# Performance work log

Measured on AMD Instinct MI355X. Metric: run time of the kernel, lower is better.

## Reference

```python
import jax, jax.numpy as jnp
import numpy as np

N, E, IN_C, HID, OUT_C, HEADS, NUM_CLASSES = 50000, 800000, 128, 64, 64, 4, 40
NEG_SLOPE = 0.2


def _gat_conv(x, src, dst, W, a_src, a_dst, bias, heads, concat):
    # x: [N, F_in]; W: [F_in, heads*C]; a_src/a_dst: [1, heads, C]; bias: [out]
    n = x.shape[0]
    h = (x @ W).reshape(n, heads, -1)                      # [N, H, C]
    alpha_s = (h * a_src).sum(-1)                          # [N, H]
    alpha_d = (h * a_dst).sum(-1)                          # [N, H]
    e = jax.nn.leaky_relu(alpha_s[src] + alpha_d[dst], NEG_SLOPE)  # [E, H]
    # scatter-softmax over incoming edges of each dst node
    emax = jax.ops.segment_max(e, dst, num_segments=n)
    emax = jnp.where(jnp.isfinite(emax), emax, 0.0)
    ee = jnp.exp(e - emax[dst])
    denom = jax.ops.segment_sum(ee, dst, num_segments=n) + 1e-16
    w = ee / denom[dst]                                    # [E, H]
    out = jax.ops.segment_sum(h[src] * w[:, :, None], dst, num_segments=n)  # [N, H, C]
    out = out.reshape(n, -1) if concat else out.mean(axis=1)
    return out + bias


def setup_inputs() -> dict:
    key = jax.random.key(0)
    ks = jax.random.split(key, 12)
    s1 = 1.0 / np.sqrt(IN_C)
    s2 = 1.0 / np.sqrt(HID * HEADS)
    s3 = 1.0 / np.sqrt(OUT_C)
    return {
        "x": jax.random.normal(ks[0], (N, IN_C), dtype=jnp.float32),
        "edge_index": jax.random.randint(ks[1], (2, E), 0, N, dtype=jnp.int64),
        "W1": jax.random.normal(ks[2], (IN_C, HEADS * HID), dtype=jnp.float32) * s1,
        "att_src1": jax.random.normal(ks[3], (1, HEADS, HID), dtype=jnp.float32) * s1,
        "att_dst1": jax.random.normal(ks[4], (1, HEADS, HID), dtype=jnp.float32) * s1,
        "b1": jnp.zeros((HEADS * HID,), dtype=jnp.float32),
        "W2": jax.random.normal(ks[5], (HEADS * HID, OUT_C), dtype=jnp.float32) * s2,
        "att_src2": jax.random.normal(ks[6], (1, 1, OUT_C), dtype=jnp.float32) * s2,
        "att_dst2": jax.random.normal(ks[7], (1, 1, OUT_C), dtype=jnp.float32) * s2,
        "b2": jnp.zeros((OUT_C,), dtype=jnp.float32),
        "fc_w": jax.random.normal(ks[8], (OUT_C, NUM_CLASSES), dtype=jnp.float32) * s3,
        "fc_b": jnp.zeros((NUM_CLASSES,), dtype=jnp.float32),
    }


def reference(x, edge_index, W1, att_src1, att_dst1, b1, W2, att_src2, att_dst2, b2, fc_w, fc_b):
    n = x.shape[0]
    loops = jnp.arange(n, dtype=edge_index.dtype)
    ei = jnp.concatenate([edge_index, jnp.stack([loops, loops])], axis=1)  # add self-loops (PyG default)
    src, dst = ei[0], ei[1]
    h = jax.nn.relu(_gat_conv(x, src, dst, W1, att_src1, att_dst1, b1, HEADS, True))
    h = jax.nn.relu(_gat_conv(h, src, dst, W2, att_src2, att_dst2, b2, 1, False))
    # dropout p=0.01 is identity in eval mode
    pooled = h.mean(axis=0, keepdims=True)                 # global mean pool -> [1, OUT_C]
    logits = pooled @ fc_w + fc_b
    return jax.nn.log_softmax(logits, axis=1)
```

## Files before the change

### kernel.cpp

```cpp
#include <hip/hip_runtime.h>
#include <hip/hip_bf16.h>
#include <math.h>

#define NEG_SLOPE 0.2f
#define CHUNK2 2048
#define PGROUPS 32

typedef __attribute__((ext_vector_type(8))) short bf16x8;
typedef __attribute__((ext_vector_type(4))) float f32x4;
typedef __attribute__((ext_vector_type(2))) float f32x2_t;

__device__ __forceinline__ float lrelu(float a) { return a >= 0.f ? a : NEG_SLOPE * a; }
__device__ __forceinline__ unsigned short f2bu(float v) {
  unsigned u = __float_as_uint(v);
  u += 0x7fffu + ((u >> 16) & 1u);
  return (unsigned short)(u >> 16);
}
__device__ __forceinline__ unsigned char f2fp8(float v) {
  return (unsigned char)(__builtin_amdgcn_cvt_pk_fp8_f32(v, v, 0, false) & 0xFF);
}

__global__ __launch_bounds__(256) void prep_kernel(
    const float* __restrict__ W1, unsigned short* __restrict__ w1t,
    const float* __restrict__ W2, unsigned short* __restrict__ w2t,
    const int* __restrict__ ei, int* __restrict__ bhist,
    int E0, int Etot, int NBUCK, int wBlocks, int histBlocks) {
  __shared__ int hsm[256];
  int t = threadIdx.x;
  if (blockIdx.x < (unsigned)wBlocks) {
    const int tot1 = 128 * 256, tot2 = 256 * 64;
    for (int i = blockIdx.x * 256 + t; i < tot1 + tot2; i += wBlocks * 256) {
      if (i < tot1) { int k = i >> 8, n = i & 255; w1t[n * 128 + k] = f2bu(W1[i]); }
      else { int j = i - tot1; int k = j >> 6, n = j & 63; w2t[n * 256 + k] = f2bu(W2[j]); }
    }
  } else {
    int bid = blockIdx.x - wBlocks;
    hsm[t] = 0;
    __syncthreads();
    for (int e = bid * 256 + t; e < Etot; e += histBlocks * 256) {
      int dst = (e < E0) ? ei[E0 + e] : (e - E0);
      atomicAdd(&hsm[dst >> 8], 1);
    }
    __syncthreads();
    if (t < NBUCK && hsm[t]) atomicAdd(&bhist[t], hsm[t]);
  }
}

__global__ __launch_bounds__(256) void bucket_scan_kernel(const int* __restrict__ bhist,
    int* __restrict__ bucketOff, int* __restrict__ cursor, int* __restrict__ rowptrN,
    float* __restrict__ pooled_grp, int NBUCK, int Etot) {
  __shared__ int s[256];
  int t = threadIdx.x;
  int v = (t < NBUCK) ? bhist[t] : 0;
  s[t] = v;
  __syncthreads();
  for (int off = 1; off < 256; off <<= 1) {
    int u = (t >= off) ? s[t - off] : 0;
    __syncthreads();
    s[t] += u;
    __syncthreads();
  }
  int excl = s[t] - v;
  if (t < NBUCK) { bucketOff[t] = excl; cursor[t] = excl; }
  if (t == 0) { bucketOff[NBUCK] = Etot; *rowptrN = Etot; }
  for (int i = t; i < PGROUPS * 64; i += 256) pooled_grp[i] = 0.f;
}

__device__ void gemm1_tile(const float* __restrict__ x,
    const unsigned short* __restrict__ BT, unsigned char* __restrict__ C8,
    const float* __restrict__ att_s, const float* __restrict__ att_d,
    float* __restrict__ as_, float* __restrict__ ad_,
    int M, int by, char* smem) {
  unsigned short (*Al)[40] = (unsigned short (*)[40])smem;
  unsigned short (*Bt)[40] = (unsigned short (*)[40])(smem + 5120);
  const int tid = threadIdx.x;
  const int row0 = by * 64;
  const int lane = tid & 63, wave = tid >> 6;
  const int l15 = lane & 15, q = lane >> 4;

  f32x4 acc[4][4] = {};
  const int rr = tid >> 2, rc = (tid & 3) * 8;

  for (int k0 = 0; k0 < 128; k0 += 32) {
    float4 v0 = make_float4(0.f, 0.f, 0.f, 0.f), v1 = v0;
    if (row0 + rr < M) {
      const float* ap = x + (size_t)(row0 + rr) * 128 + k0 + rc;
      v0 = *(const float4*)ap;
      v1 = *(const float4*)(ap + 4);
    }
    *(ushort4*)&Al[rr][rc] = make_ushort4(f2bu(v0.x), f2bu(v0.y), f2bu(v0.z), f2bu(v0.w));
    *(ushort4*)&Al[rr][rc + 4] = make_ushort4(f2bu(v1.x), f2bu(v1.y), f2bu(v1.z), f2bu(v1.w));
    {
      const ushort4* bp = (const ushort4*)(BT + (size_t)tid * 128 + k0);
#pragma unroll
      for (int i = 0; i < 8; i++) *(ushort4*)&Bt[tid][i * 4] = bp[i];
    }
    __syncthreads();
    bf16x8 af[4], bf[4];
#pragma unroll
    for (int mi = 0; mi < 4; mi++)
      af[mi] = *(const bf16x8*)&Al[mi * 16 + l15][q * 8];
#pragma unroll
    for (int ni = 0; ni < 4; ni++)
      bf[ni] = *(const bf16x8*)&Bt[wave * 64 + ni * 16 + l15][q * 8];
#pragma unroll
    for (int mi = 0; mi < 4; mi++)
#pragma unroll
      for (int ni = 0; ni < 4; ni++)
        acc[mi][ni] = __builtin_amdgcn_mfma_f32_16x16x32_bf16(af[mi], bf[ni], acc[mi][ni], 0, 0, 0);
    __syncthreads();
  }
  float atts[4], attd[4];
#pragma unroll
  for (int ni = 0; ni < 4; ni++) {
    atts[ni] = att_s[wave * 64 + ni * 16 + l15];
    attd[ni] = att_d[wave * 64 + ni * 16 + l15];
  }
#pragma unroll
  for (int mi = 0; mi < 4; mi++) {
#pragma unroll
    for (int r = 0; r < 4; r++) {
      int grow = row0 + mi * 16 + q * 4 + r;
      bool ok = grow < M;
      if (ok) {
#pragma unroll
        for (int ni = 0; ni < 4; ni++)
          C8[(size_t)grow * 256 + wave * 64 + ni * 16 + l15] = f2fp8(acc[mi][ni][r]);
      }
      float vs = acc[mi][0][r] * atts[0] + acc[mi][1][r] * atts[1]
               + acc[mi][2][r] * atts[2] + acc[mi][3][r] * atts[3];
      float vd = acc[mi][0][r] * attd[0] + acc[mi][1][r] * attd[1]
               + acc[mi][2][r] * attd[2] + acc[mi][3][r] * attd[3];
#pragma unroll
      for (int off = 1; off < 16; off <<= 1) {
        vs += __shfl_xor(vs, off);
        vd += __shfl_xor(vd, off);
      }
      if (ok && l15 == 0) {
        as_[(size_t)grow * 4 + wave] = vs;
        ad_[(size_t)grow * 4 + wave] = vd;
      }
    }
  }
}

__global__ __launch_bounds__(256) void gemm1_scatter_kernel(
    const float* __restrict__ x, const unsigned short* __restrict__ BT,
    unsigned char* __restrict__ C8, const float* __restrict__ att_s,
    const float* __restrict__ att_d, float* __restrict__ as_, float* __restrict__ ad_,
    int M, const int* __restrict__ ei, int* __restrict__ cursor, int* __restrict__ pairs,
    int E0, int Etot, int NBUCK, int NSC) {
  __shared__ __align__(16) char smem[25600];
  if (blockIdx.x < (unsigned)NSC) {
    int2* stage = (int2*)smem;
    int* h = (int*)(smem + 16384);
    int* base = (int*)(smem + 17408);
    int t = threadIdx.x;
    int e0 = blockIdx.x * CHUNK2;
    h[t] = 0;
    __syncthreads();
    int cnt = Etot - e0;
    if (cnt > CHUNK2) cnt = CHUNK2;
    for (int i = t; i < cnt; i += 256) {
      int e = e0 + i;
      int s, d;
      if (e < E0) { s = ei[e]; d = ei[E0 + e]; } else { s = d = e - E0; }
      stage[i] = make_int2((s << 8) | (d & 255), d >> 8);
      atomicAdd(&h[d >> 8], 1);
    }
    __syncthreads();
    if (t < NBUCK && h[t]) base[t] = atomicAdd(&cursor[t], h[t]);
    __syncthreads();
    for (int i = t; i < cnt; i += 256) {
      int2 p = stage[i];
      int pos = atomicAdd(&base[p.y], 1);
      pairs[pos] = p.x;
    }
  } else {
    gemm1_tile(x, BT, C8, att_s, att_d, as_, ad_, M, blockIdx.x - NSC, smem);
  }
}

__global__ __launch_bounds__(256) void csr_build_kernel(const int* __restrict__ pairs,
    const int* __restrict__ bucketOff, int* __restrict__ rowptr, int* __restrict__ csr_src,
    int N) {
  int b = blockIdx.x, t = threadIdx.x;
  int base = bucketOff[b], cnt = bucketOff[b + 1] - base;
  int n0 = b << 8;
  __shared__ int h[256];
  __shared__ int s[256];
  __shared__ int ex[256];
  h[t] = 0;
  __syncthreads();
  for (int i = t; i < cnt; i += 256) atomicAdd(&h[pairs[base + i] & 255], 1);
  __syncthreads();
  int v = h[t];
  s[t] = v;
  __syncthreads();
  for (int off = 1; off < 256; off <<= 1) {
    int u = (t >= off) ? s[t - off] : 0;
    __syncthreads();
    s[t] += u;
    __syncthreads();
  }
  ex[t] = s[t] - v;
  if (n0 + t < N) rowptr[n0 + t] = base + ex[t];
  __syncthreads();
  for (int i = t; i < cnt; i += 256) {
    int p = pairs[base + i];
    int pos = atomicAdd(&ex[p & 255], 1);
    csr_src[base + pos] = ((unsigned)p) >> 8;
  }
}

#define ACCV(W, X) do {                                                        \
    f32x2_t w2_; w2_.x = (W); w2_.y = (W);                                     \
    av[0] += w2_ * __builtin_amdgcn_cvt_pk_f32_fp8((X).x, false);              \
    av[1] += w2_ * __builtin_amdgcn_cvt_pk_f32_fp8((X).x, true);               \
    av[2] += w2_ * __builtin_amdgcn_cvt_pk_f32_fp8((X).y, false);              \
    av[3] += w2_ * __builtin_amdgcn_cvt_pk_f32_fp8((X).y, true);               \
    av[4] += w2_ * __builtin_amdgcn_cvt_pk_f32_fp8((X).z, false);              \
    av[5] += w2_ * __builtin_amdgcn_cvt_pk_f32_fp8((X).z, true);               \
    av[6] += w2_ * __builtin_amdgcn_cvt_pk_f32_fp8((X).w, false);              \
    av[7] += w2_ * __builtin_amdgcn_cvt_pk_f32_fp8((X).w, true);               \
  } while (0)

__global__ __launch_bounds__(256) void aggr1_kernel(const int* __restrict__ rowptr,
    const int* __restrict__ csr_src, const float* __restrict__ as_,
    const float* __restrict__ ad_, const uint4* __restrict__ h1f8,
    const float* __restrict__ b1, unsigned short* __restrict__ out1, int Nn) {
  int lane = threadIdx.x & 63, wv = threadIdx.x >> 6;
  int q = lane >> 4, l15 = lane & 15;
  int n = (blockIdx.x * 4 + wv) * 4 + q;
  if (n >= Nn) return;
  int row = rowptr[n], deg = rowptr[n + 1] - row;
  int hh = l15 >> 2;
  float adv = ad_[n * 4 + hh];
  const uint4* hb = h1f8 + l15;
  f32x2_t av[8] = {};
  float wsum = 0.f;
  for (int s = 0; s < deg; s += 8) {
    int id[8];
    float al[8];
    uint4 xv[8];
#pragma unroll
    for (int u = 0; u < 8; u++) {
      int p = s + u;
      if (p > deg - 1) p = deg - 1;
      id[u] = csr_src[row + p];
    }
#pragma unroll
    for (int u = 0; u < 8; u++) al[u] = as_[id[u] * 4 + hh];
#pragma unroll
    for (int u = 0; u < 8; u++) xv[u] = hb[(size_t)id[u] * 16];
#pragma unroll
    for (int u = 0; u < 8; u++) {
      float w = (s + u < deg) ? __expf(lrelu(al[u] + adv)) : 0.f;
      wsum += w;
      ACCV(w, xv[u]);
    }
  }
  float vinv = 1.f / wsum;
  int c0i = l15 * 16;
  unsigned short ob[16];
#pragma unroll
  for (int k = 0; k < 4; k++) {
    float4 bb = *(const float4*)(b1 + c0i + k * 4);
    float r0 = fmaf(av[k * 2].x, vinv, bb.x);
    float r1 = fmaf(av[k * 2].y, vinv, bb.y);
    float r2 = fmaf(av[k * 2 + 1].x, vinv, bb.z);
    float r3 = fmaf(av[k * 2 + 1].y, vinv, bb.w);
    ob[k * 4 + 0] = f2bu(r0 > 0.f ? r0 : 0.f);
    ob[k * 4 + 1] = f2bu(r1 > 0.f ? r1 : 0.f);
    ob[k * 4 + 2] = f2bu(r2 > 0.f ? r2 : 0.f);
    ob[k * 4 + 3] = f2bu(r3 > 0.f ? r3 : 0.f);
  }
  *(ushort4*)(out1 + (size_t)n * 256 + c0i) = *(ushort4*)&ob[0];
  *(ushort4*)(out1 + (size_t)n * 256 + c0i + 4) = *(ushort4*)&ob[4];
  *(ushort4*)(out1 + (size_t)n * 256 + c0i + 8) = *(ushort4*)&ob[8];
  *(ushort4*)(out1 + (size_t)n * 256 + c0i + 12) = *(ushort4*)&ob[12];
}

__global__ __launch_bounds__(256) void gemm2_kernel(const unsigned short* __restrict__ A,
    const unsigned short* __restrict__ BT, unsigned char* __restrict__ C8,
    const float* __restrict__ att_s, const float* __restrict__ att_d,
    float* __restrict__ as_, float* __restrict__ ad_, int M) {
  const int K = 256, Ncol = 64;
  __shared__ __align__(16) char smem[11264];
  unsigned short (*Al)[40] = (unsigned short (*)[40])smem;
  unsigned short (*Bt)[40] = (unsigned short (*)[40])(smem + 5120);
  float* sal = (float*)(smem + 10240);
  float* sad = (float*)(smem + 10752);
  const int tid = threadIdx.x;
  const int row0 = blockIdx.x * 64;
  const int lane = tid & 63, wave = tid >> 6;
  const int wm = wave >> 1, wn = wave & 1;
  const int l15 = lane & 15, q = lane >> 4;

  f32x4 acc[2][2] = {};
  const int rr = tid >> 2, rc = (tid & 3) * 8;

  for (int k0 = 0; k0 < K; k0 += 32) {
    ushort4 av0 = make_ushort4(0, 0, 0, 0), av1 = av0;
    if (row0 + rr < M) {
      const ushort4* ap = (const ushort4*)(A + (size_t)(row0 + rr) * K + k0 + rc);
      av0 = ap[0]; av1 = ap[1];
    }
    *(ushort4*)&Al[rr][rc] = av0;
    *(ushort4*)&Al[rr][rc + 4] = av1;
    {
      const ushort4* bp = (const ushort4*)(BT + (size_t)rr * K + k0 + rc);
      *(ushort4*)&Bt[rr][rc] = bp[0];
      *(ushort4*)&Bt[rr][rc + 4] = bp[1];
    }
    __syncthreads();
    bf16x8 af[2], bf[2];
#pragma unroll
    for (int mi = 0; mi < 2; mi++)
      af[mi] = *(const bf16x8*)&Al[wm * 32 + mi * 16 + l15][q * 8];
#pragma unroll
    for (int ni = 0; ni < 2; ni++)
      bf[ni] = *(const bf16x8*)&Bt[wn * 32 + ni * 16 + l15][q * 8];
#pragma unroll
    for (int mi = 0; mi < 2; mi++)
#pragma unroll
      for (int ni = 0; ni < 2; ni++)
        acc[mi][ni] = __builtin_amdgcn_mfma_f32_16x16x32_bf16(af[mi], bf[ni], acc[mi][ni], 0, 0, 0);
    __syncthreads();
  }
#pragma unroll
  for (int mi = 0; mi < 2; mi++) {
#pragma unroll
    for (int r = 0; r < 4; r++) {
      int grow = row0 + wm * 32 + mi * 16 + q * 4 + r;
      if (grow < M) {
#pragma unroll
        for (int ni = 0; ni < 2; ni++) {
          int gcol = wn * 32 + ni * 16 + l15;
          C8[(size_t)grow * Ncol + gcol] = f2fp8(acc[mi][ni][r]);
        }
      }
    }
  }
  float atts0 = att_s[wn * 32 + l15], atts1 = att_s[wn * 32 + 16 + l15];
  float attd0 = att_d[wn * 32 + l15], attd1 = att_d[wn * 32 + 16 + l15];
#pragma unroll
  for (int mi = 0; mi < 2; mi++) {
#pragma unroll
    for (int r = 0; r < 4; r++) {
      float vs = acc[mi][0][r] * atts0 + acc[mi][1][r] * atts1;
      float vd = acc[mi][0][r] * attd0 + acc[mi][1][r] * attd1;
#pragma unroll
      for (int off = 1; off < 16; off <<= 1) {
        vs += __shfl_xor(vs, off);
        vd += __shfl_xor(vd, off);
      }
      if (l15 == 0) {
        int rl = wm * 32 + mi * 16 + q * 4 + r;
        sal[wn * 64 + rl] = vs;
        sad[wn * 64 + rl] = vd;
      }
    }
  }
  __syncthreads();
  if (tid < 64) {
    int grow = row0 + tid;
    if (grow < M) {
      as_[grow] = sal[tid] + sal[64 + tid];
      ad_[grow] = sad[tid] + sad[64 + tid];
    }
  }
}

__global__ __launch_bounds__(256) void aggr2_pool_kernel(const int* __restrict__ rowptr,
    const int* __restrict__ csr_src, const float* __restrict__ as_,
    const float* __restrict__ ad_, const unsigned* __restrict__ h2f8,
    const float* __restrict__ b2, float* __restrict__ pooled_grp, int Nn) {
  int lane = threadIdx.x & 63, wv = threadIdx.x >> 6;
  int q = lane >> 4, l15 = lane & 15;
  int c0 = l15 * 4;
  const unsigned* hb = h2f8 + l15;
  f32x2_t pv0 = {0.f, 0.f}, pv1 = {0.f, 0.f};
  int stream = (blockIdx.x * 4 + wv) * 4 + q;
  int nstreams = gridDim.x * 16;
  for (int n = stream; n < Nn; n += nstreams) {
    int row = rowptr[n], deg = rowptr[n + 1] - row;
    float adv = ad_[n];
    f32x2_t a01 = {0.f, 0.f}, a23 = {0.f, 0.f};
    float wsum = 0.f;
    for (int s = 0; s < deg; s += 8) {
      int id[8];
      float al[8];
      unsigned xv[8];
#pragma unroll
      for (int u = 0; u < 8; u++) {
        int p = s + u;
        if (p > deg - 1) p = deg - 1;
        id[u] = csr_src[row + p];
      }
#pragma unroll
      for (int u = 0; u < 8; u++) al[u] = as_[id[u]];
#pragma unroll
      for (int u = 0; u < 8; u++) xv[u] = hb[(size_t)id[u] * 16];
#pragma unroll
      for (int u = 0; u < 8; u++) {
        float w = (s + u < deg) ? __expf(lrelu(al[u] + adv)) : 0.f;
        wsum += w;
        f32x2_t w2_; w2_.x = w; w2_.y = w;
        a01 += w2_ * __builtin_amdgcn_cvt_pk_f32_fp8(xv[u], false);
        a23 += w2_ * __builtin_amdgcn_cvt_pk_f32_fp8(xv[u], true);
      }
    }
    float vinv = 1.f / wsum;
    float4 bb = *(const float4*)(b2 + c0);
    float r0 = fmaf(a01.x, vinv, bb.x), r1 = fmaf(a01.y, vinv, bb.y);
    float r2 = fmaf(a23.x, vinv, bb.z), r3 = fmaf(a23.y, vinv, bb.w);
    pv0.x += r0 > 0.f ? r0 : 0.f; pv0.y += r1 > 0.f ? r1 : 0.f;
    pv1.x += r2 > 0.f ? r2 : 0.f; pv1.y += r3 > 0.f ? r3 : 0.f;
  }
  __shared__ float4 sred[4][4][16];
  sred[wv][q][l15] = make_float4(pv0.x, pv0.y, pv1.x, pv1.y);
  __syncthreads();
  if (threadIdx.x < 64) {
    int slot = threadIdx.x >> 2, comp = threadIdx.x & 3;
    float acc = 0.f;
#pragma unroll
    for (int i = 0; i < 4; i++)
#pragma unroll
      for (int j = 0; j < 4; j++) {
        float4 v = sred[i][j][slot];
        acc += comp == 0 ? v.x : (comp == 1 ? v.y : (comp == 2 ? v.z : v.w));
      }
    atomicAdd(&pooled_grp[(blockIdx.x & (PGROUPS - 1)) * 64 + slot * 4 + comp], acc);
  }
}

__global__ __launch_bounds__(64) void pool_head_kernel(const float* __restrict__ pooled_grp,
    const float* __restrict__ fc_w, const float* __restrict__ fc_b,
    float* __restrict__ out, float invN) {
  int t = threadIdx.x;
  __shared__ float pl[64];
  __shared__ float lg[40];
  __shared__ float lse;
  float acc = 0.f;
#pragma unroll
  for (int g = 0; g < PGROUPS; g++) acc += pooled_grp[g * 64 + t];
  pl[t] = acc * invN;
  __syncthreads();
  if (t < 40) {
    float sm = fc_b[t];
    for (int c = 0; c < 64; c++) sm = fmaf(pl[c], fc_w[c * 40 + t], sm);
    lg[t] = sm;
  }
  __syncthreads();
  if (t == 0) {
    float m = -1e30f;
    for (int j = 0; j < 40; j++) m = fmaxf(m, lg[j]);
    float su = 0.f;
    for (int j = 0; j < 40; j++) su += expf(lg[j] - m);
    lse = m + logf(su);
  }
  __syncthreads();
  if (t < 40) out[t] = lg[t] - lse;
}

extern "C" void kernel_launch(void* const* d_in, const int* in_sizes, int n_in,
                              void* d_out, int out_size, void* d_ws, size_t ws_size,
                              hipStream_t stream) {
  const float* x        = (const float*)d_in[0];
  const int*   ei       = (const int*)d_in[1];
  const float* W1       = (const float*)d_in[2];
  const float* att_src1 = (const float*)d_in[3];
  const float* att_dst1 = (const float*)d_in[4];
  const float* b1       = (const float*)d_in[5];
  const float* W2       = (const float*)d_in[6];
  const float* att_src2 = (const float*)d_in[7];
  const float* att_dst2 = (const float*)d_in[8];
  const float* b2       = (const float*)d_in[9];
  const float* fc_w     = (const float*)d_in[10];
  const float* fc_b     = (const float*)d_in[11];
  float* out = (float*)d_out;

  const int N    = in_sizes[0] / 128;
  const int E0   = in_sizes[1] / 2;
  const int Etot = E0 + N;
  const int NBUCK = (N + 255) >> 8;
  const int NSC  = (Etot + CHUNK2 - 1) / CHUNK2;
  const int GBY  = (N + 63) / 64;
  const int AGG2_BLOCKS = 2048;

  char* wsb = (char*)d_ws;
  size_t o = 0;
  auto alloc = [&](size_t bytes) { char* p = wsb + o; o += (bytes + 15) & ~(size_t)15; return p; };
  unsigned short* w1t  = (unsigned short*)alloc(256 * 128 * 2);
  unsigned short* w2t  = (unsigned short*)alloc(64 * 256 * 2);
  unsigned char*  h1f8 = (unsigned char*)alloc((size_t)N * 256);
  unsigned char*  h2   = (unsigned char*)alloc((size_t)N * 64);
  unsigned short* out1 = (unsigned short*)alloc((size_t)N * 256 * 2);
  float* as1  = (float*)alloc((size_t)N * 4 * 4);
  float* ad1  = (float*)alloc((size_t)N * 4 * 4);
  float* as2  = (float*)alloc((size_t)N * 4);
  float* ad2  = (float*)alloc((size_t)N * 4);
  int* rowptr = (int*)alloc((size_t)(N + 1) * 4);
  int* bhist  = (int*)alloc(256 * 4);
  int* bucketOff = (int*)alloc(257 * 4);
  int* cursor = (int*)alloc(256 * 4);
  int* pairs  = (int*)alloc((size_t)Etot * 4);
  int* csr_src = (int*)alloc((size_t)Etot * 4);
  float* pooled_grp = (float*)alloc((size_t)PGROUPS * 64 * 4);

  dim3 blk(256);

  hipMemsetAsync(bhist, 0, 256 * sizeof(int), stream);
  prep_kernel<<<16 + 256, blk, 0, stream>>>(W1, w1t, W2, w2t, ei, bhist,
                                            E0, Etot, NBUCK, 16, 256);
  bucket_scan_kernel<<<1, blk, 0, stream>>>(bhist, bucketOff, cursor, rowptr + N,
                                            pooled_grp, NBUCK, Etot);

  gemm1_scatter_kernel<<<NSC + GBY, blk, 0, stream>>>(
      x, w1t, h1f8, att_src1, att_dst1, as1, ad1, N,
      ei, cursor, pairs, E0, Etot, NBUCK, NSC);
  csr_build_kernel<<<NBUCK, blk, 0, stream>>>(pairs, bucketOff, rowptr, csr_src, N);

  aggr1_kernel<<<(N + 15) / 16, blk, 0, stream>>>(rowptr, csr_src, as1, ad1,
                                                  (const uint4*)h1f8, b1, out1, N);

  gemm2_kernel<<<GBY, blk, 0, stream>>>(out1, w2t, h2, att_src2, att_dst2, as2, ad2, N);
  aggr2_pool_kernel<<<AGG2_BLOCKS, blk, 0, stream>>>(rowptr, csr_src, as2, ad2,
                                                     (const unsigned*)h2, b2, pooled_grp, N);

  pool_head_kernel<<<1, 64, 0, stream>>>(pooled_grp, fc_w, fc_b, out, 1.0f / (float)N);
}
```

Before: 217.0 us.

## Build CSR directly with per-node histogram and global atomic cursors

Replaces the two-level bucket sort (bucket-staged pairs followed by a per-bucket CSR build kernel) with a per-node degree histogram in the prep kernel, a per-bucket scan kernel that produces rowptr and per-node cursors, and a direct scatter of source indices into csr_src using global atomics on the destination cursor. This removes the intermediate pairs buffer and the csr_build kernel. In exchange it adds about a million global atomics on node counters in both histogram and scatter, with scattered writes, and the order of edges within each row becomes nondeterministic.

```diff
diff --git a/kernel.cpp b/kernel.cpp
--- a/kernel.cpp
+++ b/kernel.cpp
@@ -3,7 +3,6 @@
 #include <math.h>
 
 #define NEG_SLOPE 0.2f
-#define CHUNK2 2048
 #define PGROUPS 32
 
 typedef __attribute__((ext_vector_type(8))) short bf16x8;
@@ -23,7 +22,7 @@
 __global__ __launch_bounds__(256) void prep_kernel(
     const float* __restrict__ W1, unsigned short* __restrict__ w1t,
     const float* __restrict__ W2, unsigned short* __restrict__ w2t,
-    const int* __restrict__ ei, int* __restrict__ bhist,
+    const int* __restrict__ ei, int* __restrict__ bhist, int* __restrict__ nhist,
     int E0, int Etot, int NBUCK, int wBlocks, int histBlocks) {
   __shared__ int hsm[256];
   int t = threadIdx.x;
@@ -40,6 +39,7 @@
     for (int e = bid * 256 + t; e < Etot; e += histBlocks * 256) {
       int dst = (e < E0) ? ei[E0 + e] : (e - E0);
       atomicAdd(&hsm[dst >> 8], 1);
+      atomicAdd(&nhist[dst], 1);
     }
     __syncthreads();
     if (t < NBUCK && hsm[t]) atomicAdd(&bhist[t], hsm[t]);
@@ -47,7 +47,7 @@
 }
 
 __global__ __launch_bounds__(256) void bucket_scan_kernel(const int* __restrict__ bhist,
-    int* __restrict__ bucketOff, int* __restrict__ cursor, int* __restrict__ rowptrN,
+    int* __restrict__ bucketOff, int* __restrict__ rowptrN,
     float* __restrict__ pooled_grp, int NBUCK, int Etot) {
   __shared__ int s[256];
   int t = threadIdx.x;
@@ -61,9 +61,31 @@
     __syncthreads();
   }
   int excl = s[t] - v;
-  if (t < NBUCK) { bucketOff[t] = excl; cursor[t] = excl; }
+  if (t < NBUCK) bucketOff[t] = excl;
   if (t == 0) { bucketOff[NBUCK] = Etot; *rowptrN = Etot; }
   for (int i = t; i < PGROUPS * 64; i += 256) pooled_grp[i] = 0.f;
+}
+
+__global__ __launch_bounds__(256) void rowptr_kernel(const int* __restrict__ nhist,
+    const int* __restrict__ bucketOff, int* __restrict__ rowptr, int* __restrict__ cursor,
+    int N) {
+  int b = blockIdx.x, t = threadIdx.x;
+  int n = (b << 8) + t;
+  __shared__ int s[256];
+  int v = (n < N) ? nhist[n] : 0;
+  s[t] = v;
+  __syncthreads();
+  for (int off = 1; off < 256; off <<= 1) {
+    int u = (t >= off) ? s[t - off] : 0;
+    __syncthreads();
+    s[t] += u;
+    __syncthreads();
+  }
+  if (n < N) {
+    int r = bucketOff[b] + s[t] - v;
+    rowptr[n] = r;
+    cursor[n] = r;
+  }
 }
 
 __device__ void gemm1_tile(const float* __restrict__ x,
@@ -148,68 +170,18 @@
     const float* __restrict__ x, const unsigned short* __restrict__ BT,
     unsigned char* __restrict__ C8, const float* __restrict__ att_s,
     const float* __restrict__ att_d, float* __restrict__ as_, float* __restrict__ ad_,
-    int M, const int* __restrict__ ei, int* __restrict__ cursor, int* __restrict__ pairs,
-    int E0, int Etot, int NBUCK, int NSC) {
+    int M, const int* __restrict__ ei, int* __restrict__ cursor, int* __restrict__ csr_src,
+    int E0, int Etot, int NSC) {
   __shared__ __align__(16) char smem[25600];
   if (blockIdx.x < (unsigned)NSC) {
-    int2* stage = (int2*)smem;
-    int* h = (int*)(smem + 16384);
-    int* base = (int*)(smem + 17408);
-    int t = threadIdx.x;
-    int e0 = blockIdx.x * CHUNK2;
-    h[t] = 0;
-    __syncthreads();
-    int cnt = Etot - e0;
-    if (cnt > CHUNK2) cnt = CHUNK2;
-    for (int i = t; i < cnt; i += 256) {
-      int e = e0 + i;
+    for (int e = blockIdx.x * 256 + threadIdx.x; e < Etot; e += NSC * 256) {
       int s, d;
       if (e < E0) { s = ei[e]; d = ei[E0 + e]; } else { s = d = e - E0; }
-      stage[i] = make_int2((s << 8) | (d & 255), d >> 8);
-      atomicAdd(&h[d >> 8], 1);
-    }
-    __syncthreads();
-    if (t < NBUCK && h[t]) base[t] = atomicAdd(&cursor[t], h[t]);
-    __syncthreads();
-    for (int i = t; i < cnt; i += 256) {
-      int2 p = stage[i];
-      int pos = atomicAdd(&base[p.y], 1);
-      pairs[pos] = p.x;
+      int pos = atomicAdd(&cursor[d], 1);
+      csr_src[pos] = s;
     }
   } else {
     gemm1_tile(x, BT, C8, att_s, att_d, as_, ad_, M, blockIdx.x - NSC, smem);
-  }
-}
-
-__global__ __launch_bounds__(256) void csr_build_kernel(const int* __restrict__ pairs,
-    const int* __restrict__ bucketOff, int* __restrict__ rowptr, int* __restrict__ csr_src,
-    int N) {
-  int b = blockIdx.x, t = threadIdx.x;
-  int base = bucketOff[b], cnt = bucketOff[b + 1] - base;
-  int n0 = b << 8;
-  __shared__ int h[256];
-  __shared__ int s[256];
-  __shared__ int ex[256];
-  h[t] = 0;
-  __syncthreads();
-  for (int i = t; i < cnt; i += 256) atomicAdd(&h[pairs[base + i] & 255], 1);
-  __syncthreads();
-  int v = h[t];
-  s[t] = v;
-  __syncthreads();
-  for (int off = 1; off < 256; off <<= 1) {
-    int u = (t >= off) ? s[t - off] : 0;
-    __syncthreads();
-    s[t] += u;
-    __syncthreads();
-  }
-  ex[t] = s[t] - v;
-  if (n0 + t < N) rowptr[n0 + t] = base + ex[t];
-  __syncthreads();
-  for (int i = t; i < cnt; i += 256) {
-    int p = pairs[base + i];
-    int pos = atomicAdd(&ex[p & 255], 1);
-    csr_src[base + pos] = ((unsigned)p) >> 8;
   }
 }
 
@@ -485,7 +457,7 @@
   const int E0   = in_sizes[1] / 2;
   const int Etot = E0 + N;
   const int NBUCK = (N + 255) >> 8;
-  const int NSC  = (Etot + CHUNK2 - 1) / CHUNK2;
+  const int NSC  = 128;
   const int GBY  = (N + 63) / 64;
   const int AGG2_BLOCKS = 2048;
 
@@ -502,25 +474,25 @@
   float* as2  = (float*)alloc((size_t)N * 4);
   float* ad2  = (float*)alloc((size_t)N * 4);
   int* rowptr = (int*)alloc((size_t)(N + 1) * 4);
-  int* bhist  = (int*)alloc(256 * 4);
+  int* bhist  = (int*)alloc((256 + (size_t)N) * 4);
+  int* nhist  = bhist + 256;
   int* bucketOff = (int*)alloc(257 * 4);
-  int* cursor = (int*)alloc(256 * 4);
-  int* pairs  = (int*)alloc((size_t)Etot * 4);
+  int* cursor = (int*)alloc((size_t)N * 4);
   int* csr_src = (int*)alloc((size_t)Etot * 4);
   float* pooled_grp = (float*)alloc((size_t)PGROUPS * 64 * 4);
 
   dim3 blk(256);
 
-  hipMemsetAsync(bhist, 0, 256 * sizeof(int), stream);
-  prep_kernel<<<16 + 256, blk, 0, stream>>>(W1, w1t, W2, w2t, ei, bhist,
+  hipMemsetAsync(bhist, 0, (256 + (size_t)N) * sizeof(int), stream);
+  prep_kernel<<<16 + 256, blk, 0, stream>>>(W1, w1t, W2, w2t, ei, bhist, nhist,
                                             E0, Etot, NBUCK, 16, 256);
-  bucket_scan_kernel<<<1, blk, 0, stream>>>(bhist, bucketOff, cursor, rowptr + N,
+  bucket_scan_kernel<<<1, blk, 0, stream>>>(bhist, bucketOff, rowptr + N,
                                             pooled_grp, NBUCK, Etot);
+  rowptr_kernel<<<NBUCK, blk, 0, stream>>>(nhist, bucketOff, rowptr, cursor, N);
 
   gemm1_scatter_kernel<<<NSC + GBY, blk, 0, stream>>>(
       x, w1t, h1f8, att_src1, att_dst1, as1, ad1, N,
-      ei, cursor, pairs, E0, Etot, NBUCK, NSC);
-  csr_build_kernel<<<NBUCK, blk, 0, stream>>>(pairs, bucketOff, rowptr, csr_src, N);
+      ei, cursor, csr_src, E0, Etot, NSC);
 
   aggr1_kernel<<<(N + 15) / 16, blk, 0, stream>>>(rowptr, csr_src, as1, ad1,
                                                   (const uint4*)h1f8, b1, out1, N);
```

New measurement: 249.2 us. 1.15x slower.
